# Kernel tuning notes

Measured on AMD Instinct MI355X. Metric: run time of the kernel, lower is better.

The kernel has to match this reference:

```python
import jax, jax.numpy as jnp
import numpy as np

K_NEIGHBORS = 5  # sklearn KNNImputer default n_neighbors, weights='uniform'


def _impute_feature(Xz, present):
    # Xz: [N, T1] feature values with 0 at missing entries; present: [N, T1] bool.
    # sklearn nan_euclidean distance: sqrt(T1/cnt * sum_valid (x_i - y_i)^2),
    # valid dims = both present; cnt==0 -> excluded (treated as inf here).
    T1 = Xz.shape[1]
    pf = present.astype(Xz.dtype)
    sq = Xz * Xz
    d2 = sq @ pf.T + pf @ sq.T - 2.0 * (Xz @ Xz.T)  # [N, N]
    cnt = pf @ pf.T
    d2 = jnp.maximum(d2, 0.0) * (jnp.asarray(T1, Xz.dtype) / jnp.maximum(cnt, 1.0))
    dist = jnp.sqrt(d2)
    dist = jnp.where(cnt > 0, dist, jnp.inf)
    # distances only pick neighbors (piecewise-constant wrt values)
    dist = jax.lax.stop_gradient(dist)

    def impute_col(xcol, prescol):
        # donors must have a value in this column and a finite distance
        d = jnp.where(prescol[None, :], dist, jnp.inf)  # [N, N]
        negv, idx = jax.lax.top_k(-d, K_NEIGHBORS)       # k smallest distances
        sel_ok = jnp.isfinite(negv)                      # [N, K]
        vals = xcol[idx]                                 # [N, K] donor values
        cntk = sel_ok.sum(-1)
        mean_k = (vals * sel_ok).sum(-1) / jnp.maximum(cntk, 1)
        # fallback: observed column mean when no valid donor (sklearn behavior)
        colmean = (xcol * prescol).sum() / jnp.maximum(prescol.sum(), 1)
        imput = jnp.where(cntk > 0, mean_k, colmean)
        return jnp.where(prescol, xcol, imput)  # [N]

    # vmap over the T1 columns -> [T1, N]
    return jax.vmap(impute_col, in_axes=(1, 1))(Xz, present)


def reference(x_all, mask):
    # x_all: [T1, N, D_in] stacked node features (steps + output graph)
    # mask:  [T1, N] int, 1 = missing (original code: last channel of x)
    T1, N, D_in = x_all.shape
    C = D_in - 1  # output_node_dim
    present = (mask == 0).T  # [N, T1]
    outs = []
    for c in range(C):
        X = x_all[..., c].T                      # [N, T1]
        Xz = jnp.where(present, X, 0.0)
        steps = _impute_feature(Xz, present)     # [T1, N]
        outs.append(steps[-1])                   # last step = output graph
    return jnp.stack(outs, axis=-1)              # [N, C] -> h_v


def setup_inputs() -> dict:
    key = jax.random.key(0)
    k1, k2 = jax.random.split(key)
    x_all = jax.random.normal(k1, (17, 2048, 9), dtype=jnp.float32)
    mask = jax.random.randint(k2, (17, 2048), 0, 2, dtype=jnp.int32)
    return {"x_all": x_all, "mask": mask}
```

## Files before the change

kernel.cpp:

```cpp
#include <hip/hip_runtime.h>
#include <math.h>

#define T1 17
#define NN 2048
#define DIN 9
#define CC 8
#define KK 5
#define NSTR 5
#define NDCAP (NSTR * 256)
#define NQCAP 1280
#define LPAD (NDCAP + 8)
#define NU (NDCAP / 64)
#define PLANE (NN * CC)

#define XD_BYTES (T1 * NN * CC * 4)

__global__ __launch_bounds__(128) void prep_a(
    const float* __restrict__ x_all, const int* __restrict__ mask,
    unsigned* __restrict__ pm, unsigned long long* __restrict__ wsbal,
    float* __restrict__ wscol, float* __restrict__ out) {
  const int row = blockIdx.x * 128 + threadIdx.x;
  const int lane = threadIdx.x & 63;
  const int g = row >> 6;
  unsigned m = 0;
#pragma unroll
  for (int t = 0; t < T1; ++t)
    m |= (mask[t * NN + row] == 0 ? 1u : 0u) << t;
  pm[row] = m;
  const bool v = (m >> 16) & 1u;
  const unsigned long long bal = __ballot(v);

  float s[CC];
#pragma unroll
  for (int c = 0; c < CC; ++c) s[c] = 0.f;
  if (v) {
    const float* r = x_all + ((size_t)16 * NN + row) * DIN;
#pragma unroll
    for (int c = 0; c < CC; ++c) {
      const float vv = r[c];
      s[c] = vv;
      out[row * CC + c] = vv;
    }
  }
#pragma unroll
  for (int off = 32; off > 0; off >>= 1) {
#pragma unroll
    for (int c = 0; c < CC; ++c) s[c] += __shfl_down(s[c], off);
  }
  if (lane == 0) {
    wsbal[g] = bal;
#pragma unroll
    for (int c = 0; c < CC; ++c) wscol[g * CC + c] = s[c];
  }
}

__global__ __launch_bounds__(1024) void prep_b(
    const unsigned* __restrict__ pm, const unsigned long long* __restrict__ wsbal,
    const float* __restrict__ wscol, int* __restrict__ dlist,
    unsigned* __restrict__ pmd, int* __restrict__ qlist,
    float* __restrict__ colmean, int* __restrict__ cnts) {
  __shared__ int dpre[33], qpre[33];
  __shared__ unsigned long long sbal[32];
  const int tid = threadIdx.x;
  if (tid < 32) sbal[tid] = wsbal[tid];
  __syncthreads();
  if (tid == 0) {
    int a = 0, b = 0;
    for (int g = 0; g < 32; ++g) {
      dpre[g] = a;
      qpre[g] = b;
      const int p = (int)__popcll(sbal[g]);
      a += p;
      b += 64 - p;
    }
    dpre[32] = a;
    qpre[32] = b;
    cnts[0] = a;
    cnts[1] = b;
  }
  __syncthreads();
#pragma unroll
  for (int h = 0; h < 2; ++h) {
    const int row = tid + h * 1024;
    const unsigned m = pm[row];
    const int g = row >> 6, l = row & 63;
    const unsigned long long bal = sbal[g];
    const unsigned long long ltm = (1ull << l) - 1ull;
    if ((m >> 16) & 1u) {
      const int p = dpre[g] + (int)__popcll(bal & ltm);
      dlist[p] = row;
      pmd[p] = m;
    } else {
      const int p = qpre[g] + (int)__popcll((~bal) & ltm);
      qlist[p] = row;
    }
  }
  if (tid < CC) {
    float tot = 0.f;
#pragma unroll
    for (int g = 0; g < 32; ++g) tot += wscol[g * CC + tid];
    colmean[tid] = tot / fmaxf((float)dpre[32], 1.f);
  }
}

__global__ void transpose_kernel(const float* __restrict__ x_all,
                                 const int* __restrict__ dlist,
                                 const int* __restrict__ cnts,
                                 float* __restrict__ xd) {
  const int u = blockIdx.x * 256 + threadIdx.x;
  if (u >= T1 * NN * CC) return;
  const int t = u / (NN * CC);
  const int rem = u % (NN * CC);
  const int dn = rem >> 3;
  const int c = rem & 7;
  if (dn < cnts[0]) xd[u] = x_all[((size_t)t * NN + dlist[dn]) * DIN + c];
}

__global__ __launch_bounds__(512, 3) void knn_main(
    const float* __restrict__ x_all, const float* __restrict__ xd,
    const unsigned* __restrict__ pm, const unsigned* __restrict__ pmd,
    const int* __restrict__ qlist, const int* __restrict__ cnts,
    const float* __restrict__ colmean, float* __restrict__ out) {
  __shared__ float sdist[CC][LPAD];
  __shared__ float qlds[T1][CC];
  __shared__ float rcp17[32];
  const int nq = cnts[1];
  const int bid = blockIdx.x;
  if (bid >= nq) return;
  const int i = qlist[bid];
  const int ndon = cnts[0];
  const unsigned mi = (unsigned)__builtin_amdgcn_readfirstlane((int)pm[i]);
  const int tid = threadIdx.x;

  if (tid < 32) rcp17[tid] = 17.f / (float)tid;
  if (tid < 16 * CC)
    qlds[tid >> 3][tid & 7] = x_all[((size_t)(tid >> 3) * NN + i) * DIN + (tid & 7)];
  if (tid >= 16 * CC && tid < 17 * CC) qlds[16][tid & 7] = 0.f;
  __syncthreads();

  const int qd = tid & 1;
  const int c0 = qd * 4;
  const int dg = tid >> 1;
  const int lane = tid & 63;
  const int w = tid >> 6;

  float a0[NSTR], a1[NSTR], a2[NSTR], a3[NSTR];
  unsigned ms[NSTR];
  int eoff[NSTR];
#pragma unroll
  for (int s = 0; s < NSTR; ++s) {
    const int dn = dg + 256 * s;
    ms[s] = (dn < ndon) ? (mi & pmd[dn]) : 0u;
    eoff[s] = dn * CC + c0;
    a0[s] = a1[s] = a2[s] = a3[s] = 0.f;
  }

  unsigned tm = mi & 0xFFFFu;
  while (tm) {
    const int t0 = __ffs(tm) - 1;
    tm &= tm - 1u;
    int t1 = 16;
    if (tm) { t1 = __ffs(tm) - 1; tm &= tm - 1u; }
    const float* __restrict__ p0 = xd + (size_t)t0 * PLANE;
    const float* __restrict__ p1 = xd + (size_t)t1 * PLANE;
    const float4 qv0 = *(const float4*)&qlds[t0][c0];
    const float4 qv1 = *(const float4*)&qlds[t1][c0];
#pragma unroll
    for (int s = 0; s < NSTR; ++s) {
      if (ms[s]) {
        const float4 dv0 = *(const float4*)(p0 + eoff[s]);
        const float4 dv1 = *(const float4*)(p1 + eoff[s]);
        const float fl0 = (float)((ms[s] >> t0) & 1u);
        const float fl1 = (float)((ms[s] >> t1) & 1u);
        float e;
        e = qv0.x - dv0.x; a0[s] = fmaf(e * e, fl0, a0[s]);
        e = qv0.y - dv0.y; a1[s] = fmaf(e * e, fl0, a1[s]);
        e = qv0.z - dv0.z; a2[s] = fmaf(e * e, fl0, a2[s]);
        e = qv0.w - dv0.w; a3[s] = fmaf(e * e, fl0, a3[s]);
        e = qv1.x - dv1.x; a0[s] = fmaf(e * e, fl1, a0[s]);
        e = qv1.y - dv1.y; a1[s] = fmaf(e * e, fl1, a1[s]);
        e = qv1.z - dv1.z; a2[s] = fmaf(e * e, fl1, a2[s]);
        e = qv1.w - dv1.w; a3[s] = fmaf(e * e, fl1, a3[s]);
      }
    }
  }

#pragma unroll
  for (int s = 0; s < NSTR; ++s) {
    const int dn = dg + 256 * s;
    const int cnt = __popc(ms[s]);
    const float sc = rcp17[cnt & 31];
    const bool ok = cnt > 0;
    sdist[c0 + 0][dn] = ok ? sqrtf(a0[s] * sc) : INFINITY;
    sdist[c0 + 1][dn] = ok ? sqrtf(a1[s] * sc) : INFINITY;
    sdist[c0 + 2][dn] = ok ? sqrtf(a2[s] * sc) : INFINITY;
    sdist[c0 + 3][dn] = ok ? sqrtf(a3[s] * sc) : INFINITY;
  }
  __syncthreads();

  float dvr[NU];
#pragma unroll
  for (int u = 0; u < NU; ++u) dvr[u] = sdist[w][u * 64 + lane];

  float sum = 0.f;
  int cn = 0;
#pragma unroll
  for (int k = 0; k < KK; ++k) {
    float g = dvr[0];
#pragma unroll
    for (int u = 1; u < NU; ++u) g = fminf(g, dvr[u]);
#pragma unroll
    for (int off = 32; off > 0; off >>= 1) g = fminf(g, __shfl_xor(g, off));
    if (g < INFINITY) {
      int jloc = 0x7FFFFFFF;
#pragma unroll
      for (int u = NU - 1; u >= 0; --u)
        if (dvr[u] == g) jloc = u * 64 + lane;
      int jg = jloc;
#pragma unroll
      for (int off = 32; off > 0; off >>= 1) jg = min(jg, __shfl_xor(jg, off));
      const int jgs = __builtin_amdgcn_readfirstlane(jg);
      const int tu = jgs >> 6, tl = jgs & 63;
#pragma unroll
      for (int u = 0; u < NU; ++u)
        if (u == tu) dvr[u] = (lane == tl) ? INFINITY : dvr[u];
      sum += xd[((size_t)16 * NN + jgs) * CC + w];
      ++cn;
    }
  }
  if (lane == 0) out[i * CC + w] = (cn > 0) ? sum / (float)cn : colmean[w];
}

extern "C" void kernel_launch(void* const* d_in, const int* in_sizes, int n_in,
                              void* d_out, int out_size, void* d_ws, size_t ws_size,
                              hipStream_t stream) {
  const float* x_all = (const float*)d_in[0];
  const int* mask = (const int*)d_in[1];
  float* out = (float*)d_out;

  char* ws = (char*)d_ws;
  float* xd = (float*)ws;
  unsigned* pm = (unsigned*)(ws + XD_BYTES);
  int* dlist = (int*)(ws + XD_BYTES + NN * 4);
  unsigned* pmd = (unsigned*)(ws + XD_BYTES + NN * 8);
  int* qlist = (int*)(ws + XD_BYTES + NN * 12);
  float* colmean = (float*)(ws + XD_BYTES + NN * 16);
  int* cnts = (int*)(ws + XD_BYTES + NN * 16 + CC * 4);
  unsigned long long* wsbal = (unsigned long long*)(ws + XD_BYTES + NN * 16 + CC * 4 + 64);
  float* wscol = (float*)(ws + XD_BYTES + NN * 16 + CC * 4 + 64 + 32 * 8);

  prep_a<<<16, 128, 0, stream>>>(x_all, mask, pm, wsbal, wscol, out);
  prep_b<<<1, 1024, 0, stream>>>(pm, wsbal, wscol, dlist, pmd, qlist, colmean, cnts);
  transpose_kernel<<<(T1 * NN * CC + 255) / 256, 256, 0, stream>>>(x_all, dlist, cnts, xd);
  knn_main<<<NQCAP, 512, 0, stream>>>(x_all, xd, pm, pmd, qlist, cnts, colmean, out);
}
```

Baseline: 46.30 us.

## Batch four queries per block with double-buffered LDS donor tiles

Each block now handles four query rows, one per wavefront, instead of one query per 512-thread block. Donor feature tiles of 64 donors by 16 steps by 8 channels are staged into double-buffered shared memory, so each global load is shared by four queries and the next tile's load overlaps the current tile's compute. Distances for all 8 channels are kept in registers per lane, so top-k selection needs no shared-memory distance array, and missing dimensions are masked with a bit-and instead of a float multiply. The cost is much higher register pressure (160 distance registers per lane), a barrier per tile, and per-step loops whose trip count differs between waves.

```diff
diff --git a/kernel.cpp b/kernel.cpp
--- a/kernel.cpp
+++ b/kernel.cpp
@@ -6,13 +6,11 @@
 #define DIN 9
 #define CC 8
 #define KK 5
-#define NSTR 5
-#define NDCAP (NSTR * 256)
+#define QB 4
+#define NT 20
+#define NDCAP (NT * 64)
 #define NQCAP 1280
-#define LPAD (NDCAP + 8)
-#define NU (NDCAP / 64)
-#define PLANE (NN * CC)
-
+#define PLANEF (NN * CC)
 #define XD_BYTES (T1 * NN * CC * 4)
 
 __global__ __launch_bounds__(128) void prep_a(
@@ -116,119 +114,173 @@
   if (dn < cnts[0]) xd[u] = x_all[((size_t)t * NN + dlist[dn]) * DIN + c];
 }
 
-__global__ __launch_bounds__(512, 3) void knn_main(
+__global__ __launch_bounds__(256, 2) void knn_main(
     const float* __restrict__ x_all, const float* __restrict__ xd,
     const unsigned* __restrict__ pm, const unsigned* __restrict__ pmd,
     const int* __restrict__ qlist, const int* __restrict__ cnts,
     const float* __restrict__ colmean, float* __restrict__ out) {
-  __shared__ float sdist[CC][LPAD];
-  __shared__ float qlds[T1][CC];
+  __shared__ float tb[2][16 * 64 * CC];
+  __shared__ float qlds[QB][16][CC];
   __shared__ float rcp17[32];
   const int nq = cnts[1];
   const int bid = blockIdx.x;
-  if (bid >= nq) return;
-  const int i = qlist[bid];
+  if (bid * QB >= nq) return;
   const int ndon = cnts[0];
-  const unsigned mi = (unsigned)__builtin_amdgcn_readfirstlane((int)pm[i]);
   const int tid = threadIdx.x;
-
-  if (tid < 32) rcp17[tid] = 17.f / (float)tid;
-  if (tid < 16 * CC)
-    qlds[tid >> 3][tid & 7] = x_all[((size_t)(tid >> 3) * NN + i) * DIN + (tid & 7)];
-  if (tid >= 16 * CC && tid < 17 * CC) qlds[16][tid & 7] = 0.f;
-  __syncthreads();
-
-  const int qd = tid & 1;
-  const int c0 = qd * 4;
-  const int dg = tid >> 1;
   const int lane = tid & 63;
   const int w = tid >> 6;
-
-  float a0[NSTR], a1[NSTR], a2[NSTR], a3[NSTR];
-  unsigned ms[NSTR];
-  int eoff[NSTR];
-#pragma unroll
-  for (int s = 0; s < NSTR; ++s) {
-    const int dn = dg + 256 * s;
-    ms[s] = (dn < ndon) ? (mi & pmd[dn]) : 0u;
-    eoff[s] = dn * CC + c0;
-    a0[s] = a1[s] = a2[s] = a3[s] = 0.f;
-  }
-
-  unsigned tm = mi & 0xFFFFu;
-  while (tm) {
-    const int t0 = __ffs(tm) - 1;
-    tm &= tm - 1u;
-    int t1 = 16;
-    if (tm) { t1 = __ffs(tm) - 1; tm &= tm - 1u; }
-    const float* __restrict__ p0 = xd + (size_t)t0 * PLANE;
-    const float* __restrict__ p1 = xd + (size_t)t1 * PLANE;
-    const float4 qv0 = *(const float4*)&qlds[t0][c0];
-    const float4 qv1 = *(const float4*)&qlds[t1][c0];
-#pragma unroll
-    for (int s = 0; s < NSTR; ++s) {
-      if (ms[s]) {
-        const float4 dv0 = *(const float4*)(p0 + eoff[s]);
-        const float4 dv1 = *(const float4*)(p1 + eoff[s]);
-        const float fl0 = (float)((ms[s] >> t0) & 1u);
-        const float fl1 = (float)((ms[s] >> t1) & 1u);
-        float e;
-        e = qv0.x - dv0.x; a0[s] = fmaf(e * e, fl0, a0[s]);
-        e = qv0.y - dv0.y; a1[s] = fmaf(e * e, fl0, a1[s]);
-        e = qv0.z - dv0.z; a2[s] = fmaf(e * e, fl0, a2[s]);
-        e = qv0.w - dv0.w; a3[s] = fmaf(e * e, fl0, a3[s]);
-        e = qv1.x - dv1.x; a0[s] = fmaf(e * e, fl1, a0[s]);
-        e = qv1.y - dv1.y; a1[s] = fmaf(e * e, fl1, a1[s]);
-        e = qv1.z - dv1.z; a2[s] = fmaf(e * e, fl1, a2[s]);
-        e = qv1.w - dv1.w; a3[s] = fmaf(e * e, fl1, a3[s]);
-      }
-    }
-  }
-
-#pragma unroll
-  for (int s = 0; s < NSTR; ++s) {
-    const int dn = dg + 256 * s;
-    const int cnt = __popc(ms[s]);
-    const float sc = rcp17[cnt & 31];
-    const bool ok = cnt > 0;
-    sdist[c0 + 0][dn] = ok ? sqrtf(a0[s] * sc) : INFINITY;
-    sdist[c0 + 1][dn] = ok ? sqrtf(a1[s] * sc) : INFINITY;
-    sdist[c0 + 2][dn] = ok ? sqrtf(a2[s] * sc) : INFINITY;
-    sdist[c0 + 3][dn] = ok ? sqrtf(a3[s] * sc) : INFINITY;
-  }
+  const int qidx = bid * QB + w;
+  const bool qok = qidx < nq;
+  const int i = qlist[qok ? qidx : bid * QB];
+  const unsigned mi = (unsigned)__builtin_amdgcn_readfirstlane((int)pm[i]);
+
+  if (tid < 32) rcp17[tid] = 17.f / (float)tid;
+#pragma unroll
+  for (int h = tid; h < QB * 16 * CC; h += 256) {
+    const int q = h >> 7, t = (h >> 3) & 15, c = h & 7;
+    const int qq = bid * QB + q;
+    const int iq = (qq < nq) ? qlist[qq] : qlist[bid * QB];
+    qlds[q][t][c] = x_all[((size_t)t * NN + iq) * DIN + c];
+  }
+
+  const int thalf = tid >> 7;
+  const int ip = tid & 127;
+  const int ssw = (ip * 4) ^ ((tid & 8) >> 1);
+  const int lp = ip * 4;
+  const int swr = lane & 4;
+
+  float d0[NT], d1[NT], d2[NT], d3[NT], d4[NT], d5[NT], d6[NT], d7[NT];
+#pragma unroll
+  for (int u = 0; u < NT; ++u) {
+    d0[u] = INFINITY; d1[u] = INFINITY; d2[u] = INFINITY; d3[u] = INFINITY;
+    d4[u] = INFINITY; d5[u] = INFINITY; d6[u] = INFINITY; d7[u] = INFINITY;
+  }
+
+  float4 sv0, sv1, sv2, sv3, sv4, sv5, sv6, sv7;
+
+#define STAGE_LOAD(U)                                                        \
+  {                                                                          \
+    const float* sb = xd + (size_t)(U) * 512 + ssw;                          \
+    sv0 = *(const float4*)(sb + (size_t)(0 + thalf) * PLANEF);               \
+    sv1 = *(const float4*)(sb + (size_t)(2 + thalf) * PLANEF);               \
+    sv2 = *(const float4*)(sb + (size_t)(4 + thalf) * PLANEF);               \
+    sv3 = *(const float4*)(sb + (size_t)(6 + thalf) * PLANEF);               \
+    sv4 = *(const float4*)(sb + (size_t)(8 + thalf) * PLANEF);               \
+    sv5 = *(const float4*)(sb + (size_t)(10 + thalf) * PLANEF);              \
+    sv6 = *(const float4*)(sb + (size_t)(12 + thalf) * PLANEF);              \
+    sv7 = *(const float4*)(sb + (size_t)(14 + thalf) * PLANEF);              \
+  }
+
+#define STAGE_WRITE(BUF)                                                     \
+  {                                                                          \
+    float* wb = &tb[BUF][thalf * 512 + lp];                                  \
+    *(float4*)(wb + 0 * 1024) = sv0;                                         \
+    *(float4*)(wb + 1 * 1024) = sv1;                                         \
+    *(float4*)(wb + 2 * 1024) = sv2;                                         \
+    *(float4*)(wb + 3 * 1024) = sv3;                                         \
+    *(float4*)(wb + 4 * 1024) = sv4;                                         \
+    *(float4*)(wb + 5 * 1024) = sv5;                                         \
+    *(float4*)(wb + 6 * 1024) = sv6;                                         \
+    *(float4*)(wb + 7 * 1024) = sv7;                                         \
+  }
+
+#define COMPUTE(U, BUF)                                                      \
+  {                                                                          \
+    const int dn = (U) * 64 + lane;                                          \
+    const unsigned mk = (dn < ndon) ? (mi & pmd[dn]) : 0u;                   \
+    float a0 = 0.f, a1 = 0.f, a2 = 0.f, a3 = 0.f;                            \
+    float a4 = 0.f, a5 = 0.f, a6 = 0.f, a7 = 0.f;                            \
+    unsigned tm = mi & 0xFFFFu;                                              \
+    while (tm) {                                                             \
+      const int t = __ffs(tm) - 1;                                           \
+      tm &= tm - 1u;                                                         \
+      const int em = ((int)(mk << (31 - t))) >> 31;                          \
+      const float4 qv0 = *(const float4*)&qlds[w][t][0];                     \
+      const float4 qv1 = *(const float4*)&qlds[w][t][4];                     \
+      const float* db = &tb[BUF][t * 512 + lane * 8];                        \
+      const float4 dv0 = *(const float4*)(db + swr);                         \
+      const float4 dv1 = *(const float4*)(db + (4 ^ swr));                   \
+      float e;                                                               \
+      e = qv0.x - dv0.x; e = __int_as_float(__float_as_int(e) & em); a0 = fmaf(e, e, a0); \
+      e = qv0.y - dv0.y; e = __int_as_float(__float_as_int(e) & em); a1 = fmaf(e, e, a1); \
+      e = qv0.z - dv0.z; e = __int_as_float(__float_as_int(e) & em); a2 = fmaf(e, e, a2); \
+      e = qv0.w - dv0.w; e = __int_as_float(__float_as_int(e) & em); a3 = fmaf(e, e, a3); \
+      e = qv1.x - dv1.x; e = __int_as_float(__float_as_int(e) & em); a4 = fmaf(e, e, a4); \
+      e = qv1.y - dv1.y; e = __int_as_float(__float_as_int(e) & em); a5 = fmaf(e, e, a5); \
+      e = qv1.z - dv1.z; e = __int_as_float(__float_as_int(e) & em); a6 = fmaf(e, e, a6); \
+      e = qv1.w - dv1.w; e = __int_as_float(__float_as_int(e) & em); a7 = fmaf(e, e, a7); \
+    }                                                                        \
+    const int cnt = __popc(mk);                                              \
+    const float sc = rcp17[cnt & 31];                                        \
+    const bool ok = cnt > 0;                                                 \
+    d0[U] = ok ? sqrtf(a0 * sc) : INFINITY;                                  \
+    d1[U] = ok ? sqrtf(a1 * sc) : INFINITY;                                  \
+    d2[U] = ok ? sqrtf(a2 * sc) : INFINITY;                                  \
+    d3[U] = ok ? sqrtf(a3 * sc) : INFINITY;                                  \
+    d4[U] = ok ? sqrtf(a4 * sc) : INFINITY;                                  \
+    d5[U] = ok ? sqrtf(a5 * sc) : INFINITY;                                  \
+    d6[U] = ok ? sqrtf(a6 * sc) : INFINITY;                                  \
+    d7[U] = ok ? sqrtf(a7 * sc) : INFINITY;                                  \
+  }
+
+#define TILE(U)                                                              \
+  if ((U) * 64 < ndon) {                                                     \
+    if (((U) + 1) < NT && ((U) + 1) * 64 < ndon) STAGE_LOAD((U) + 1);        \
+    COMPUTE(U, (U) & 1);                                                     \
+    if (((U) + 1) < NT && ((U) + 1) * 64 < ndon) {                           \
+      STAGE_WRITE(((U) + 1) & 1);                                            \
+      __syncthreads();                                                       \
+    }                                                                        \
+  }
+
+  STAGE_LOAD(0);
+  STAGE_WRITE(0);
   __syncthreads();
 
-  float dvr[NU];
-#pragma unroll
-  for (int u = 0; u < NU; ++u) dvr[u] = sdist[w][u * 64 + lane];
-
-  float sum = 0.f;
-  int cn = 0;
-#pragma unroll
-  for (int k = 0; k < KK; ++k) {
-    float g = dvr[0];
-#pragma unroll
-    for (int u = 1; u < NU; ++u) g = fminf(g, dvr[u]);
-#pragma unroll
-    for (int off = 32; off > 0; off >>= 1) g = fminf(g, __shfl_xor(g, off));
-    if (g < INFINITY) {
-      int jloc = 0x7FFFFFFF;
-#pragma unroll
-      for (int u = NU - 1; u >= 0; --u)
-        if (dvr[u] == g) jloc = u * 64 + lane;
-      int jg = jloc;
-#pragma unroll
-      for (int off = 32; off > 0; off >>= 1) jg = min(jg, __shfl_xor(jg, off));
-      const int jgs = __builtin_amdgcn_readfirstlane(jg);
-      const int tu = jgs >> 6, tl = jgs & 63;
-#pragma unroll
-      for (int u = 0; u < NU; ++u)
-        if (u == tu) dvr[u] = (lane == tl) ? INFINITY : dvr[u];
-      sum += xd[((size_t)16 * NN + jgs) * CC + w];
-      ++cn;
-    }
-  }
-  if (lane == 0) out[i * CC + w] = (cn > 0) ? sum / (float)cn : colmean[w];
+  TILE(0); TILE(1); TILE(2); TILE(3); TILE(4);
+  TILE(5); TILE(6); TILE(7); TILE(8); TILE(9);
+  TILE(10); TILE(11); TILE(12); TILE(13); TILE(14);
+  TILE(15); TILE(16); TILE(17); TILE(18); TILE(19);
+
+  const float* __restrict__ xd16 = xd + (size_t)16 * PLANEF;
+
+#define SELECT_CH(DC, CIDX)                                                  \
+  {                                                                          \
+    float sum = 0.f;                                                         \
+    int cn = 0;                                                              \
+    for (int k = 0; k < KK; ++k) {                                           \
+      float g = DC[0];                                                       \
+      _Pragma("unroll")                                                      \
+      for (int u = 1; u < NT; ++u) g = fminf(g, DC[u]);                      \
+      _Pragma("unroll")                                                      \
+      for (int off = 32; off > 0; off >>= 1) g = fminf(g, __shfl_xor(g, off)); \
+      if (!(g < INFINITY)) break;                                            \
+      int jloc = 0x7FFFFFFF;                                                 \
+      _Pragma("unroll")                                                      \
+      for (int u = NT - 1; u >= 0; --u)                                      \
+        if (DC[u] == g) jloc = u * 64 + lane;                                \
+      _Pragma("unroll")                                                      \
+      for (int off = 32; off > 0; off >>= 1) jloc = min(jloc, __shfl_xor(jloc, off)); \
+      const int jgs = __builtin_amdgcn_readfirstlane(jloc);                  \
+      const int tu = jgs >> 6, tl = jgs & 63;                                \
+      _Pragma("unroll")                                                      \
+      for (int u = 0; u < NT; ++u)                                           \
+        if (u == tu) DC[u] = (lane == tl) ? INFINITY : DC[u];                \
+      sum += xd16[jgs * CC + (CIDX)];                                        \
+      ++cn;                                                                  \
+    }                                                                        \
+    if (qok && lane == 0)                                                    \
+      out[i * CC + (CIDX)] = (cn > 0) ? sum / (float)cn : colmean[(CIDX)];   \
+  }
+
+  SELECT_CH(d0, 0);
+  SELECT_CH(d1, 1);
+  SELECT_CH(d2, 2);
+  SELECT_CH(d3, 3);
+  SELECT_CH(d4, 4);
+  SELECT_CH(d5, 5);
+  SELECT_CH(d6, 6);
+  SELECT_CH(d7, 7);
 }
 
 extern "C" void kernel_launch(void* const* d_in, const int* in_sizes, int n_in,
@@ -252,5 +304,5 @@
   prep_a<<<16, 128, 0, stream>>>(x_all, mask, pm, wsbal, wscol, out);
   prep_b<<<1, 1024, 0, stream>>>(pm, wsbal, wscol, dlist, pmd, qlist, colmean, cnts);
   transpose_kernel<<<(T1 * NN * CC + 255) / 256, 256, 0, stream>>>(x_all, dlist, cnts, xd);
-  knn_main<<<NQCAP, 512, 0, stream>>>(x_all, xd, pm, pmd, qlist, cnts, colmean, out);
-}
+  knn_main<<<NQCAP / QB, 256, 0, stream>>>(x_all, xd, pm, pmd, qlist, cnts, colmean, out);
+}
```

Result: slower. 90.83 us (+96.2%).

## Restructure KNN as per-lane query tiles with register top-5 and merge kernel

Applied to the files above, without the earlier changes.

Replaces one-block-per-query distance computation and wavefront-wide argmin selection with a layout where each lane owns one query and loops over a 64-donor split, keeping a running sorted top-5 in registers for two channels. Partial top-5 lists from 20 donor splits are written to workspace and merged by a new kernel that averages the donor values. This drops the LDS distance buffer and the repeated cross-lane reductions, and reuses each donor load across 64 queries. The cost is an extra launch, workspace traffic for the partial lists, branchy insertion code, and all 16 timesteps evaluated through masking rather than skipped.

```diff
diff --git a/kernel.cpp b/kernel.cpp
--- a/kernel.cpp
+++ b/kernel.cpp
@@ -6,14 +6,18 @@
 #define DIN 9
 #define CC 8
 #define KK 5
-#define NSTR 5
-#define NDCAP (NSTR * 256)
-#define NQCAP 1280
-#define LPAD (NDCAP + 8)
-#define NU (NDCAP / 64)
-#define PLANE (NN * CC)
-
+#define QCAP 1280
+#define NQG 20
+#define NSP 20
+#define NDCAP (NSP * 64)
+#define NCP 4
+#define PLANEF (NN * CC)
 #define XD_BYTES (T1 * NN * CC * 4)
+#define MAXJ 0x7FFFFFFF
+
+__device__ __forceinline__ bool lexlt(float d1, int j1, float d2, int j2) {
+  return d1 < d2 || (d1 == d2 && j1 < j2);
+}
 
 __global__ __launch_bounds__(128) void prep_a(
     const float* __restrict__ x_all, const int* __restrict__ mask,
@@ -116,119 +120,141 @@
   if (dn < cnts[0]) xd[u] = x_all[((size_t)t * NN + dlist[dn]) * DIN + c];
 }
 
-__global__ __launch_bounds__(512, 3) void knn_main(
+#define INS(D, JN, D0, D1, D2, D3, D4, J0, J1, J2, J3, J4)                   \
+  if ((D) < D4) {                                                            \
+    D4 = (D); J4 = (JN);                                                     \
+    if (D4 < D3) { float tf_ = D3; D3 = D4; D4 = tf_; int ti_ = J3; J3 = J4; J4 = ti_; } \
+    if (D3 < D2) { float tf_ = D2; D2 = D3; D3 = tf_; int ti_ = J2; J2 = J3; J3 = ti_; } \
+    if (D2 < D1) { float tf_ = D1; D1 = D2; D2 = tf_; int ti_ = J1; J1 = J2; J2 = ti_; } \
+    if (D1 < D0) { float tf_ = D0; D0 = D1; D1 = tf_; int ti_ = J0; J0 = J1; J1 = ti_; } \
+  }
+
+__global__ __launch_bounds__(256) void knn_main(
     const float* __restrict__ x_all, const float* __restrict__ xd,
     const unsigned* __restrict__ pm, const unsigned* __restrict__ pmd,
     const int* __restrict__ qlist, const int* __restrict__ cnts,
-    const float* __restrict__ colmean, float* __restrict__ out) {
-  __shared__ float sdist[CC][LPAD];
-  __shared__ float qlds[T1][CC];
+    float* __restrict__ dpl, int* __restrict__ jpl) {
+  __shared__ float qlds[2][16][64];
   __shared__ float rcp17[32];
-  const int nq = cnts[1];
+  const int nq = __builtin_amdgcn_readfirstlane(cnts[1]);
+  const int nd0 = __builtin_amdgcn_readfirstlane(cnts[0]);
+  const int nd = nd0 < NDCAP ? nd0 : NDCAP;
   const int bid = blockIdx.x;
-  if (bid >= nq) return;
-  const int i = qlist[bid];
-  const int ndon = cnts[0];
-  const unsigned mi = (unsigned)__builtin_amdgcn_readfirstlane((int)pm[i]);
+  const int qg = bid / (NCP * 5);
+  const int rr = bid % (NCP * 5);
+  const int cp = rr / 5;
+  const int spg = rr % 5;
+  if (qg * 64 >= nq) return;
   const int tid = threadIdx.x;
+  const int lane = tid & 63;
+  const int w = __builtin_amdgcn_readfirstlane(tid >> 6);
+  const int sp = spg * 4 + w;
+  const int c0 = cp * 2;
 
   if (tid < 32) rcp17[tid] = 17.f / (float)tid;
-  if (tid < 16 * CC)
-    qlds[tid >> 3][tid & 7] = x_all[((size_t)(tid >> 3) * NN + i) * DIN + (tid & 7)];
-  if (tid >= 16 * CC && tid < 17 * CC) qlds[16][tid & 7] = 0.f;
+#pragma unroll
+  for (int u = 0; u < 8; ++u) {
+    const int h = tid + u * 256;
+    const int c = h >> 10, t = (h >> 6) & 15, q = h & 63;
+    int qi = qg * 64 + q;
+    if (qi >= nq) qi = nq - 1;
+    qlds[c][t][q] = x_all[((size_t)t * NN + qlist[qi]) * DIN + c0 + c];
+  }
   __syncthreads();
 
-  const int qd = tid & 1;
-  const int c0 = qd * 4;
-  const int dg = tid >> 1;
+  const int myq = qg * 64 + lane;
+  const unsigned mi = (myq < nq) ? pm[qlist[myq]] : 0u;
+
+  float qr0[16], qr1[16];
+#pragma unroll
+  for (int t = 0; t < 16; ++t) {
+    qr0[t] = qlds[0][t][lane];
+    qr1[t] = qlds[1][t][lane];
+  }
+
+  float dA0 = INFINITY, dA1 = INFINITY, dA2 = INFINITY, dA3 = INFINITY, dA4 = INFINITY;
+  float dB0 = INFINITY, dB1 = INFINITY, dB2 = INFINITY, dB3 = INFINITY, dB4 = INFINITY;
+  int jA0 = MAXJ, jA1 = MAXJ, jA2 = MAXJ, jA3 = MAXJ, jA4 = MAXJ;
+  int jB0 = MAXJ, jB1 = MAXJ, jB2 = MAXJ, jB3 = MAXJ, jB4 = MAXJ;
+
+  const int spbase = sp * 64;
+  for (int dd = 0; dd < 64; ++dd) {
+    const int dn = spbase + dd;
+    if (dn >= nd) break;
+    const unsigned pv = pmd[dn];
+    const unsigned mk = mi & pv;
+    float a0 = 0.f, a1 = 0.f;
+#pragma unroll
+    for (int t = 0; t < 16; ++t) {
+      const float2 dv = *(const float2*)&xd[(size_t)t * PLANEF + dn * CC + c0];
+      const int em = ((int)(mk << (31 - t))) >> 31;
+      float e;
+      e = qr0[t] - dv.x; e = __int_as_float(__float_as_int(e) & em); a0 = fmaf(e, e, a0);
+      e = qr1[t] - dv.y; e = __int_as_float(__float_as_int(e) & em); a1 = fmaf(e, e, a1);
+    }
+    const int cnt = __popc(mk);
+    if (cnt > 0) {
+      const float sc = rcp17[cnt];
+      const float da = sqrtf(a0 * sc);
+      INS(da, dn, dA0, dA1, dA2, dA3, dA4, jA0, jA1, jA2, jA3, jA4);
+      const float db = sqrtf(a1 * sc);
+      INS(db, dn, dB0, dB1, dB2, dB3, dB4, jB0, jB1, jB2, jB3, jB4);
+    }
+  }
+
+  const int col = qg * 64 + lane;
+#define ST(CH, K, DV, JV)                                       \
+  dpl[(((CH) * NSP + sp) * KK + (K)) * QCAP + col] = DV;        \
+  jpl[(((CH) * NSP + sp) * KK + (K)) * QCAP + col] = JV;
+  ST(c0, 0, dA0, jA0); ST(c0, 1, dA1, jA1); ST(c0, 2, dA2, jA2);
+  ST(c0, 3, dA3, jA3); ST(c0, 4, dA4, jA4);
+  ST(c0 + 1, 0, dB0, jB0); ST(c0 + 1, 1, dB1, jB1); ST(c0 + 1, 2, dB2, jB2);
+  ST(c0 + 1, 3, dB3, jB3); ST(c0 + 1, 4, dB4, jB4);
+#undef ST
+}
+
+__global__ __launch_bounds__(256) void knn_merge(
+    const float* __restrict__ xd, const int* __restrict__ qlist,
+    const int* __restrict__ cnts, const float* __restrict__ colmean,
+    const float* __restrict__ dpl, const int* __restrict__ jpl,
+    float* __restrict__ out) {
+  const int nq = __builtin_amdgcn_readfirstlane(cnts[1]);
+  const int tid = threadIdx.x;
   const int lane = tid & 63;
-  const int w = tid >> 6;
-
-  float a0[NSTR], a1[NSTR], a2[NSTR], a3[NSTR];
-  unsigned ms[NSTR];
-  int eoff[NSTR];
-#pragma unroll
-  for (int s = 0; s < NSTR; ++s) {
-    const int dn = dg + 256 * s;
-    ms[s] = (dn < ndon) ? (mi & pmd[dn]) : 0u;
-    eoff[s] = dn * CC + c0;
-    a0[s] = a1[s] = a2[s] = a3[s] = 0.f;
-  }
-
-  unsigned tm = mi & 0xFFFFu;
-  while (tm) {
-    const int t0 = __ffs(tm) - 1;
-    tm &= tm - 1u;
-    int t1 = 16;
-    if (tm) { t1 = __ffs(tm) - 1; tm &= tm - 1u; }
-    const float* __restrict__ p0 = xd + (size_t)t0 * PLANE;
-    const float* __restrict__ p1 = xd + (size_t)t1 * PLANE;
-    const float4 qv0 = *(const float4*)&qlds[t0][c0];
-    const float4 qv1 = *(const float4*)&qlds[t1][c0];
-#pragma unroll
-    for (int s = 0; s < NSTR; ++s) {
-      if (ms[s]) {
-        const float4 dv0 = *(const float4*)(p0 + eoff[s]);
-        const float4 dv1 = *(const float4*)(p1 + eoff[s]);
-        const float fl0 = (float)((ms[s] >> t0) & 1u);
-        const float fl1 = (float)((ms[s] >> t1) & 1u);
-        float e;
-        e = qv0.x - dv0.x; a0[s] = fmaf(e * e, fl0, a0[s]);
-        e = qv0.y - dv0.y; a1[s] = fmaf(e * e, fl0, a1[s]);
-        e = qv0.z - dv0.z; a2[s] = fmaf(e * e, fl0, a2[s]);
-        e = qv0.w - dv0.w; a3[s] = fmaf(e * e, fl0, a3[s]);
-        e = qv1.x - dv1.x; a0[s] = fmaf(e * e, fl1, a0[s]);
-        e = qv1.y - dv1.y; a1[s] = fmaf(e * e, fl1, a1[s]);
-        e = qv1.z - dv1.z; a2[s] = fmaf(e * e, fl1, a2[s]);
-        e = qv1.w - dv1.w; a3[s] = fmaf(e * e, fl1, a3[s]);
+  const int w = __builtin_amdgcn_readfirstlane(tid >> 6);
+  const int wt = blockIdx.x * 4 + w;
+  const int qg = wt >> 3, ch = wt & 7;
+  if (qg * 64 >= nq) return;
+  const int q = qg * 64 + lane;
+
+  float m0 = INFINITY, m1 = INFINITY, m2 = INFINITY, m3 = INFINITY, m4 = INFINITY;
+  int n0 = MAXJ, n1 = MAXJ, n2 = MAXJ, n3 = MAXJ, n4 = MAXJ;
+#pragma unroll
+  for (int sp = 0; sp < NSP; ++sp) {
+#pragma unroll
+    for (int k = 0; k < KK; ++k) {
+      const int e = ((ch * NSP + sp) * KK + k) * QCAP + q;
+      const float dv = dpl[e];
+      const int jv = jpl[e];
+      if (dv < INFINITY && lexlt(dv, jv, m4, n4)) {
+        m4 = dv; n4 = jv;
+        if (lexlt(m4, n4, m3, n3)) { float tf = m3; m3 = m4; m4 = tf; int ti = n3; n3 = n4; n4 = ti; }
+        if (lexlt(m3, n3, m2, n2)) { float tf = m2; m2 = m3; m3 = tf; int ti = n2; n2 = n3; n3 = ti; }
+        if (lexlt(m2, n2, m1, n1)) { float tf = m1; m1 = m2; m2 = tf; int ti = n1; n1 = n2; n2 = ti; }
+        if (lexlt(m1, n1, m0, n0)) { float tf = m0; m0 = m1; m1 = tf; int ti = n0; n0 = n1; n1 = ti; }
       }
     }
   }
 
-#pragma unroll
-  for (int s = 0; s < NSTR; ++s) {
-    const int dn = dg + 256 * s;
-    const int cnt = __popc(ms[s]);
-    const float sc = rcp17[cnt & 31];
-    const bool ok = cnt > 0;
-    sdist[c0 + 0][dn] = ok ? sqrtf(a0[s] * sc) : INFINITY;
-    sdist[c0 + 1][dn] = ok ? sqrtf(a1[s] * sc) : INFINITY;
-    sdist[c0 + 2][dn] = ok ? sqrtf(a2[s] * sc) : INFINITY;
-    sdist[c0 + 3][dn] = ok ? sqrtf(a3[s] * sc) : INFINITY;
-  }
-  __syncthreads();
-
-  float dvr[NU];
-#pragma unroll
-  for (int u = 0; u < NU; ++u) dvr[u] = sdist[w][u * 64 + lane];
-
+  const float* __restrict__ xd16 = xd + (size_t)16 * PLANEF;
   float sum = 0.f;
   int cn = 0;
-#pragma unroll
-  for (int k = 0; k < KK; ++k) {
-    float g = dvr[0];
-#pragma unroll
-    for (int u = 1; u < NU; ++u) g = fminf(g, dvr[u]);
-#pragma unroll
-    for (int off = 32; off > 0; off >>= 1) g = fminf(g, __shfl_xor(g, off));
-    if (g < INFINITY) {
-      int jloc = 0x7FFFFFFF;
-#pragma unroll
-      for (int u = NU - 1; u >= 0; --u)
-        if (dvr[u] == g) jloc = u * 64 + lane;
-      int jg = jloc;
-#pragma unroll
-      for (int off = 32; off > 0; off >>= 1) jg = min(jg, __shfl_xor(jg, off));
-      const int jgs = __builtin_amdgcn_readfirstlane(jg);
-      const int tu = jgs >> 6, tl = jgs & 63;
-#pragma unroll
-      for (int u = 0; u < NU; ++u)
-        if (u == tu) dvr[u] = (lane == tl) ? INFINITY : dvr[u];
-      sum += xd[((size_t)16 * NN + jgs) * CC + w];
-      ++cn;
-    }
-  }
-  if (lane == 0) out[i * CC + w] = (cn > 0) ? sum / (float)cn : colmean[w];
+  if (m0 < INFINITY) { sum += xd16[n0 * CC + ch]; ++cn; }
+  if (m1 < INFINITY) { sum += xd16[n1 * CC + ch]; ++cn; }
+  if (m2 < INFINITY) { sum += xd16[n2 * CC + ch]; ++cn; }
+  if (m3 < INFINITY) { sum += xd16[n3 * CC + ch]; ++cn; }
+  if (m4 < INFINITY) { sum += xd16[n4 * CC + ch]; ++cn; }
+  if (q < nq) out[qlist[q] * CC + ch] = (cn > 0) ? sum / (float)cn : colmean[ch];
 }
 
 extern "C" void kernel_launch(void* const* d_in, const int* in_sizes, int n_in,
@@ -248,9 +274,12 @@
   int* cnts = (int*)(ws + XD_BYTES + NN * 16 + CC * 4);
   unsigned long long* wsbal = (unsigned long long*)(ws + XD_BYTES + NN * 16 + CC * 4 + 64);
   float* wscol = (float*)(ws + XD_BYTES + NN * 16 + CC * 4 + 64 + 32 * 8);
+  float* dpl = (float*)(ws + (16 << 20));
+  int* jpl = (int*)(ws + (24 << 20));
 
   prep_a<<<16, 128, 0, stream>>>(x_all, mask, pm, wsbal, wscol, out);
   prep_b<<<1, 1024, 0, stream>>>(pm, wsbal, wscol, dlist, pmd, qlist, colmean, cnts);
   transpose_kernel<<<(T1 * NN * CC + 255) / 256, 256, 0, stream>>>(x_all, dlist, cnts, xd);
-  knn_main<<<NQCAP, 512, 0, stream>>>(x_all, xd, pm, pmd, qlist, cnts, colmean, out);
-}
+  knn_main<<<NQG * NCP * 5, 256, 0, stream>>>(x_all, xd, pm, pmd, qlist, cnts, dpl, jpl);
+  knn_merge<<<NQG * CC / 4, 256, 0, stream>>>(xd, qlist, cnts, colmean, dpl, jpl, out);
+}
```

Result: slower. 152.7 us (+229.7%).
